# Kernel optimization log

Measured on AMD Instinct MI355X. Metric: run time of the kernel, lower is better.

Reference implementation:

```python
import jax, jax.numpy as jnp
import numpy as np

H = 2048  # hidden
D = 4     # bbox dims
B, T, TGT = 64, 128, 64


def lstm_cell(x, h, c, Wih, Whh, bih, bhh):
    # PyTorch gate order: i, f, g, o
    gates = x @ Wih.T + h @ Whh.T + bih + bhh  # (B, 4H)
    i, f, g, o = jnp.split(gates, 4, axis=-1)
    i = jax.nn.sigmoid(i)
    f = jax.nn.sigmoid(f)
    g = jnp.tanh(g)
    o = jax.nn.sigmoid(o)
    c_new = f * c + i * g
    h_new = o * jnp.tanh(c_new)
    return h_new, c_new


def setup_inputs() -> dict:
    key = jax.random.key(0)
    ks = jax.random.split(key, 16)
    x = jax.random.normal(ks[0], (B, T, D), dtype=jnp.float32)
    lengths = jax.random.randint(ks[1], (B,), 1, T + 1)  # valid lengths in [1, T]
    s = 1.0 / np.sqrt(H)

    def u(k, shape):
        return jax.random.uniform(k, shape, jnp.float32, -s, s)

    return dict(
        x=x, lengths=lengths, target_len=TGT,
        enc_Wih=u(ks[2], (4 * H, D)), enc_Whh=u(ks[3], (4 * H, H)),
        enc_bih=u(ks[4], (4 * H,)), enc_bhh=u(ks[5], (4 * H,)),
        emb_W=u(ks[6], (H, D)), emb_b=u(ks[7], (H,)),
        dec_Wih=u(ks[8], (4 * H, H)), dec_Whh=u(ks[9], (4 * H, H)),
        dec_bih=u(ks[10], (4 * H,)), dec_bhh=u(ks[11], (4 * H,)),
        fc_W=u(ks[12], (D, H)), fc_b=u(ks[13], (D,)),
    )


def reference(x, lengths, target_len,
              enc_Wih, enc_Whh, enc_bih, enc_bhh,
              emb_W, emb_b,
              dec_Wih, dec_Whh, dec_bih, dec_bhh,
              fc_W, fc_b):
    b, t, _ = x.shape
    # --- Encoder: LSTM over padded seq; packed semantics = freeze state past length ---
    mask = (jnp.arange(t)[:, None] < lengths[None, :])[:, :, None]  # (T, B, 1)
    xs = jnp.swapaxes(x, 0, 1)  # (T, B, D)
    h0 = jnp.zeros((b, H), x.dtype)
    c0 = jnp.zeros((b, H), x.dtype)

    def enc_step(carry, inp):
        h, c = carry
        xt, m = inp
        hn, cn = lstm_cell(xt, h, c, enc_Wih, enc_Whh, enc_bih, enc_bhh)
        return (jnp.where(m, hn, h), jnp.where(m, cn, c)), None

    (h, c), _ = jax.lax.scan(enc_step, (h0, c0), (xs, mask))

    x0 = x[jnp.arange(b), lengths - 1]  # (B, D)

    def dec_step(carry, _):
        xb, hh, cc = carry
        emb = xb @ emb_W.T + emb_b  # (B, H)
        hh, cc = lstm_cell(emb, hh, cc, dec_Wih, dec_Whh, dec_bih, dec_bhh)
        out = hh @ fc_W.T + fc_b  # (B, D)
        return (out, hh, cc), out

    (out, h, c), preds = jax.lax.scan(dec_step, (x0, h, c), None, length=target_len)
    predictions = jnp.swapaxes(preds, 0, 1)  # (B, target_len, D)
    # hidden returned with num_layers=1 leading axis, matching torch
    return predictions, out, (h[None], c[None])
```

## Files before the change

### kernel.cpp

```cpp
#include <hip/hip_runtime.h>
#include <hip/hip_fp16.h>


#define HID   2048
#define NBAT  64
#define TENC  128
#define TDEC  64
#define NBLK  256
#define NTHR  512
#define WROW  2056
#define FROW  2056

typedef _Float16 f16;
typedef _Float16 f16x8 __attribute__((ext_vector_type(8)));
typedef _Float16 f16x4 __attribute__((ext_vector_type(4)));
typedef float    f32x4v __attribute__((ext_vector_type(4)));

#define SMEM_BYTES 159936

#define DOT4(a,b) ((a).x*(b).x + (a).y*(b).y + (a).z*(b).z + (a).w*(b).w)

struct Params {
  const float* x; const int* lengths;
  const float* enc_Wih; const float* enc_Whh; const float* enc_bih; const float* enc_bhh;
  const float* emb_W; const float* emb_b;
  const float* dec_Wih; const float* dec_Whh; const float* dec_bih; const float* dec_bhh;
  const float* fc_W; const float* fc_b;
  float* dst;
  f16* h16;
  unsigned* bar;
  int ring;
};

__device__ __forceinline__ void astore_u64(f16* p, unsigned long long v) {
  __hip_atomic_store((unsigned long long*)p, v, __ATOMIC_RELAXED, __HIP_MEMORY_SCOPE_AGENT);
}
__device__ __forceinline__ f16x8 bload_f16x8(const f16* p) {
  f16x8 r;
  asm volatile("global_load_dwordx4 %0, %1, off sc0 sc1" : "=v"(r) : "v"(p));
  return r;
}
__device__ __forceinline__ void ldsbar() {
  asm volatile("s_waitcnt lgkmcnt(0)" ::: "memory");
  __builtin_amdgcn_s_barrier();
}
__device__ __forceinline__ void waitpa() {
  asm volatile("s_waitcnt vmcnt(0)" ::: "memory");
  __builtin_amdgcn_sched_barrier(0);
}

__device__ __forceinline__ void wait_slice(const unsigned* bar, int kq, int l,
                                           unsigned level) {
  const unsigned* slot = bar + (kq << 6) + l;
  for (;;) {
    unsigned v;
    asm volatile("global_load_dword %0, %1, off sc0 sc1\n\ts_waitcnt vmcnt(0)"
                 : "=v"(v) : "v"(slot) : "memory");
    if (v >= level) break;
    __builtin_amdgcn_s_sleep(1);
  }
}
__device__ __forceinline__ void arrive(unsigned* bar, int bid, unsigned level) {
  asm volatile("s_waitcnt vmcnt(0)" ::: "memory");
  asm volatile("global_store_dword %0, %1, off sc0 sc1\n\ts_waitcnt vmcnt(0)"
               :: "v"(bar + bid), "v"(level) : "memory");
}

__device__ __forceinline__ void fill_weights(const float* __restrict__ W, int bid,
                                             f16* wlds, int w, int l) {
  #pragma unroll
  for (int rr = 0; rr < 4; ++rr) {
    int r  = w * 4 + rr;
    int gr = ((r >> 3) << 11) + bid * 8 + (r & 7);
    const float4* src = (const float4*)(W + (size_t)gr * HID);
    f16* dst = wlds + (size_t)r * WROW;
    #pragma unroll
    for (int it = 0; it < 8; ++it) {
      float4 v = src[it * 64 + l];
      f16x4 h4; h4[0] = (f16)v.x; h4[1] = (f16)v.y; h4[2] = (f16)v.z; h4[3] = (f16)v.w;
      *(f16x4*)(dst + (it * 64 + l) * 4) = h4;
    }
  }
}

__device__ __forceinline__ void gemm_prefetch(const f16* __restrict__ hp, int ring,
                                              int w, int l15, int quad,
                                              f16x8* pa0, f16x8* pa1) {
  const int mh = w & 1, kq = w >> 1;
  const f16* A0 = hp + ((size_t)(kq * 64 + quad)) * 512 + (size_t)(mh * 32 + l15) * 8;
  if (ring) {
    #pragma unroll
    for (int ch = 0; ch < 16; ++ch) {
      pa0[ch] = *(const f16x8*)(A0 + ch * 2048);
      pa1[ch] = *(const f16x8*)(A0 + ch * 2048 + 128);
    }
  } else {
    #pragma unroll
    for (int ch = 0; ch < 16; ++ch) {
      pa0[ch] = bload_f16x8(A0 + ch * 2048);
      pa1[ch] = bload_f16x8(A0 + ch * 2048 + 128);
    }
  }
}

__device__ __forceinline__ void fc_compute(const f16* fcT, float* fcp,
                                           int w, int l15, int quad,
                                           const f16x8* pa0, const f16x8* pa1) {
  const int mh = w & 1, kq = w >> 1;
  f32x4v f0 = {0.f, 0.f, 0.f, 0.f}, f1 = f0;
  const f16* BF = fcT + (size_t)l15 * FROW + kq * 512 + quad * 8;
  #pragma unroll
  for (int ch = 0; ch < 16; ++ch) {
    f16x8 vbF = {};
    if (l15 < 4) vbF = *(const f16x8*)(BF + ch * 32);
    f0 = __builtin_amdgcn_mfma_f32_16x16x32_f16(pa0[ch], vbF, f0, 0, 0, 0);
    f1 = __builtin_amdgcn_mfma_f32_16x16x32_f16(pa1[ch], vbF, f1, 0, 0, 0);
  }
  if (l15 < 4) {
    const int brow = mh * 32 + quad * 4;
    #pragma unroll
    for (int r = 0; r < 4; ++r) {
      unsafeAtomicAdd(&fcp[(brow + r) * 4 + l15],      f0[r]);
      unsafeAtomicAdd(&fcp[(brow + 16 + r) * 4 + l15], f1[r]);
    }
  }
}

template<bool FC>
__device__ __forceinline__ void gemm_compute(const f16* wlds, const f16* fcT,
                                             float* gbuf, float* fcp,
                                             int w, int l15, int quad,
                                             const f16x8* pa0, const f16x8* pa1) {
  const int mh = w & 1, kq = w >> 1;
  f32x4v a00 = {0.f, 0.f, 0.f, 0.f}, a01 = a00, a10 = a00, a11 = a00;
  const f16* B0 = wlds + (size_t)l15 * WROW + kq * 512 + quad * 8;
  const f16* B1 = B0 + (size_t)16 * WROW;
  #pragma unroll
  for (int ch = 0; ch < 16; ++ch) {
    f16x8 vb0 = *(const f16x8*)(B0 + ch * 32);
    f16x8 vb1 = *(const f16x8*)(B1 + ch * 32);
    a00 = __builtin_amdgcn_mfma_f32_16x16x32_f16(pa0[ch], vb0, a00, 0, 0, 0);
    a01 = __builtin_amdgcn_mfma_f32_16x16x32_f16(pa0[ch], vb1, a01, 0, 0, 0);
    a10 = __builtin_amdgcn_mfma_f32_16x16x32_f16(pa1[ch], vb0, a10, 0, 0, 0);
    a11 = __builtin_amdgcn_mfma_f32_16x16x32_f16(pa1[ch], vb1, a11, 0, 0, 0);
  }
  const int brow = mh * 32 + quad * 4;
  #pragma unroll
  for (int r = 0; r < 4; ++r) {
    unsafeAtomicAdd(&gbuf[(brow + r)      * 36 +      l15], a00[r]);
    unsafeAtomicAdd(&gbuf[(brow + r)      * 36 + 16 + l15], a01[r]);
    unsafeAtomicAdd(&gbuf[(brow + 16 + r) * 36 +      l15], a10[r]);
    unsafeAtomicAdd(&gbuf[(brow + 16 + r) * 36 + 16 + l15], a11[r]);
  }
  if (FC) fc_compute(fcT, fcp, w, l15, quad, pa0, pa1);
}

extern "C" __global__ void __launch_bounds__(NTHR, 2)
lstm_persistent(Params P) {
  extern __shared__ char smem[];
  f16*   wlds = (f16*)smem;
  float* gbuf = (float*)(smem + 131584);
  float* xv   = (float*)(smem + 140800);
  float* wsm  = (float*)(smem + 141824);
  float* bsm  = (float*)(smem + 142336);
  float* fcp  = (float*)(smem + 142464);
  f16*   fcT  = (f16*)(smem + 143488);

  const int t    = threadIdx.x;
  const int bid  = blockIdx.x;
  const int w    = t >> 6;
  const int l    = t & 63;
  const int l15  = l & 15;
  const int quad = l >> 4;
  const int kq   = w >> 1;
  const int bb   = t >> 3;
  const int jj   = t & 7;
  const int jglob = bid * 8 + jj;
  const int ring = P.ring;
  const size_t GEN = (size_t)NBAT * HID;

  if (t == 0)
    asm volatile("s_waitcnt vmcnt(0)\n\tbuffer_inv sc0 sc1\n\ts_waitcnt vmcnt(0)" ::: "memory");
  __syncthreads();

  if (t < 32) {
    int r = t, gr = ((r >> 3) << 11) + bid * 8 + (r & 7);
    ((float4*)wsm)[r] = ((const float4*)P.enc_Wih)[gr];
    bsm[r] = P.enc_bih[gr] + P.enc_bhh[gr];
  }
  fill_weights(P.enc_Whh, bid, wlds, w, l);

  const int len_b = P.lengths[bb];
  const float4 fcb = ((const float4*)P.fc_b)[0];
  float hreg = 0.f, creg = 0.f;

  for (int ts = 0; ts < TENC; ++ts) {
    const size_t roff = (size_t)(ring ? ts : (ts & 1)) * GEN;
    const size_t woff = (size_t)(ring ? (ts + 1) : ((ts + 1) & 1)) * GEN;
    float4 xvv;
    if (t < NBAT) xvv = ((const float4*)P.x)[t * TENC + ts];
    for (int e = t; e < 2048; e += NTHR) {
      int b = e >> 5, n = e & 31;
      gbuf[b * 36 + n] = bsm[n];
    }
    if (t < NBAT) ((float4*)xv)[t] = xvv;
    ldsbar();
    if (ts > 0) {
      wait_slice(P.bar, kq, l, (unsigned)ts);
      f16x8 pa0[16], pa1[16];
      gemm_prefetch(P.h16 + roff, ring, w, l15, quad, pa0, pa1);
      if (!ring) waitpa();
      gemm_compute<false>(wlds, fcT, gbuf, fcp, w, l15, quad, pa0, pa1);
    }
    ldsbar();
    {
      const float4 xb  = ((const float4*)xv)[bb];
      const float4 wi4 = ((const float4*)wsm)[jj];
      const float4 wf4 = ((const float4*)wsm)[8 + jj];
      const float4 wg4 = ((const float4*)wsm)[16 + jj];
      const float4 wo4 = ((const float4*)wsm)[24 + jj];
      float gi = gbuf[bb * 36 + jj]      + DOT4(xb, wi4);
      float gf = gbuf[bb * 36 + 8 + jj]  + DOT4(xb, wf4);
      float gg = gbuf[bb * 36 + 16 + jj] + DOT4(xb, wg4);
      float go = gbuf[bb * 36 + 24 + jj] + DOT4(xb, wo4);
      float ii = 1.f / (1.f + expf(-gi));
      float ff = 1.f / (1.f + expf(-gf));
      float g  = tanhf(gg);
      float oo = 1.f / (1.f + expf(-go));
      float cn = ff * creg + ii * g;
      float hn = oo * tanhf(cn);
      if (ts < len_b) { creg = cn; hreg = hn; }
      unsigned hv = (unsigned)__builtin_bit_cast(unsigned short, (f16)hreg);
      unsigned v1 = __shfl_down(hv, 1), v2 = __shfl_down(hv, 2), v3 = __shfl_down(hv, 3);
      if ((t & 3) == 0) {
        unsigned long long pk = (unsigned long long)hv | ((unsigned long long)v1 << 16)
                              | ((unsigned long long)v2 << 32) | ((unsigned long long)v3 << 48);
        astore_u64(P.h16 + woff + (size_t)bid * 512 + (size_t)bb * 8 + (jj & 4), pk);
      }
    }
    __syncthreads();
    if (t == 0) arrive(P.bar, bid, (unsigned)(ts + 1));
  }

  fill_weights(P.dec_Whh, bid, wlds, w, l);
  #pragma unroll
  for (int rr = 0; rr < 4; ++rr) {
    int r = w * 4 + rr, gr = ((r >> 3) << 11) + bid * 8 + (r & 7);
    const float* wr = P.dec_Wih + (size_t)gr * HID;
    float a0 = 0.f, a1 = 0.f, a2 = 0.f, a3 = 0.f, ab = 0.f;
    for (int k = l; k < HID; k += 64) {
      float wv = wr[k];
      float4 e = ((const float4*)P.emb_W)[k];
      a0 += wv * e.x; a1 += wv * e.y; a2 += wv * e.z; a3 += wv * e.w;
      ab += wv * P.emb_b[k];
    }
    #pragma unroll
    for (int off = 32; off > 0; off >>= 1) {
      a0 += __shfl_xor(a0, off); a1 += __shfl_xor(a1, off);
      a2 += __shfl_xor(a2, off); a3 += __shfl_xor(a3, off);
      ab += __shfl_xor(ab, off);
    }
    if (l == 0) {
      wsm[r * 4 + 0] = a0; wsm[r * 4 + 1] = a1; wsm[r * 4 + 2] = a2; wsm[r * 4 + 3] = a3;
      bsm[r] = ab + P.dec_bih[gr] + P.dec_bhh[gr];
    }
  }
  for (int i = t; i < 2048; i += NTHR) {
    int d = i >> 9, k4 = i & 511;
    float4 v = ((const float4*)P.fc_W)[i];
    f16x4 h4; h4[0] = (f16)v.x; h4[1] = (f16)v.y; h4[2] = (f16)v.z; h4[3] = (f16)v.w;
    *(f16x4*)(fcT + (size_t)d * FROW + k4 * 4) = h4;
  }
  ldsbar();

  for (int s = 0; s < TDEC; ++s) {
    const int rgen = TENC + s, wgen = rgen + 1;
    const size_t roff = (size_t)(ring ? rgen : (rgen & 1)) * GEN;
    const size_t woff = (size_t)(ring ? wgen : (wgen & 1)) * GEN;
    if (t < 256) fcp[t] = 0.f;
    for (int e = t; e < 2048; e += NTHR) {
      int b = e >> 5, n = e & 31;
      gbuf[b * 36 + n] = bsm[n];
    }
    ldsbar();
    wait_slice(P.bar, kq, l, (unsigned)rgen);
    f16x8 pa0[16], pa1[16];
    gemm_prefetch(P.h16 + roff, ring, w, l15, quad, pa0, pa1);
    if (!ring) waitpa();
    gemm_compute<true>(wlds, fcT, gbuf, fcp, w, l15, quad, pa0, pa1);
    ldsbar();
    if (t < NBAT) {
      float4 o;
      if (s == 0) {
        o = ((const float4*)P.x)[t * TENC + (P.lengths[t] - 1)];
      } else {
        float4 p = ((const float4*)fcp)[t];
        o.x = fcb.x + p.x; o.y = fcb.y + p.y; o.z = fcb.z + p.z; o.w = fcb.w + p.w;
      }
      ((float4*)xv)[t] = o;
      if (s >= 1 && bid == s)
        ((float4*)P.dst)[t * TDEC + (s - 1)] = o;
    }
    ldsbar();
    {
      const float4 xb  = ((const float4*)xv)[bb];
      const float4 wi4 = ((const float4*)wsm)[jj];
      const float4 wf4 = ((const float4*)wsm)[8 + jj];
      const float4 wg4 = ((const float4*)wsm)[16 + jj];
      const float4 wo4 = ((const float4*)wsm)[24 + jj];
      float gi = gbuf[bb * 36 + jj]      + DOT4(xb, wi4);
      float gf = gbuf[bb * 36 + 8 + jj]  + DOT4(xb, wf4);
      float gg = gbuf[bb * 36 + 16 + jj] + DOT4(xb, wg4);
      float go = gbuf[bb * 36 + 24 + jj] + DOT4(xb, wo4);
      float ii = 1.f / (1.f + expf(-gi));
      float ff = 1.f / (1.f + expf(-gf));
      float g  = tanhf(gg);
      float oo = 1.f / (1.f + expf(-go));
      creg = ff * creg + ii * g;
      hreg = oo * tanhf(creg);
      unsigned hv = (unsigned)__builtin_bit_cast(unsigned short, (f16)hreg);
      unsigned v1 = __shfl_down(hv, 1), v2 = __shfl_down(hv, 2), v3 = __shfl_down(hv, 3);
      if ((t & 3) == 0) {
        unsigned long long pk = (unsigned long long)hv | ((unsigned long long)v1 << 16)
                              | ((unsigned long long)v2 << 32) | ((unsigned long long)v3 << 48);
        astore_u64(P.h16 + woff + (size_t)bid * 512 + (size_t)bb * 8 + (jj & 4), pk);
      }
    }
    __syncthreads();
    if (t == 0) arrive(P.bar, bid, (unsigned)wgen);
  }

  if (bid == 0) {
    wait_slice(P.bar, kq, l, (unsigned)(TENC + TDEC));
    if (t < 256) fcp[t] = 0.f;
    f16x8 pa0[16], pa1[16];
    gemm_prefetch(P.h16 + (size_t)(ring ? (TENC + TDEC) : ((TENC + TDEC) & 1)) * GEN,
                  ring, w, l15, quad, pa0, pa1);
    ldsbar();
    waitpa();
    fc_compute(fcT, fcp, w, l15, quad, pa0, pa1);
    ldsbar();
    if (t < NBAT) {
      float4 p = ((const float4*)fcp)[t];
      float4 o;
      o.x = fcb.x + p.x; o.y = fcb.y + p.y; o.z = fcb.z + p.z; o.w = fcb.w + p.w;
      ((float4*)P.dst)[t * TDEC + 63] = o;
      ((float4*)(P.dst + 16384))[t]   = o;
    }
  }
  P.dst[16640  + (size_t)bb * HID + jglob] = hreg;
  P.dst[147712 + (size_t)bb * HID + jglob] = creg;
}

extern "C" void kernel_launch(void* const* d_in, const int* in_sizes, int n_in,
                              void* d_out, int out_size, void* d_ws, size_t ws_size,
                              hipStream_t stream) {
  (void)in_sizes; (void)n_in; (void)out_size;
  Params P;
  P.x        = (const float*)d_in[0];
  P.lengths  = (const int*)  d_in[1];
  P.enc_Wih  = (const float*)d_in[3];
  P.enc_Whh  = (const float*)d_in[4];
  P.enc_bih  = (const float*)d_in[5];
  P.enc_bhh  = (const float*)d_in[6];
  P.emb_W    = (const float*)d_in[7];
  P.emb_b    = (const float*)d_in[8];
  P.dec_Wih  = (const float*)d_in[9];
  P.dec_Whh  = (const float*)d_in[10];
  P.dec_bih  = (const float*)d_in[11];
  P.dec_bhh  = (const float*)d_in[12];
  P.fc_W     = (const float*)d_in[13];
  P.fc_b     = (const float*)d_in[14];
  P.dst      = (float*)d_out;

  char* ws = (char*)d_ws;
  const size_t slot = (size_t)NBAT * HID * sizeof(_Float16);
  const size_t ring_bytes = (size_t)(TENC + TDEC + 1) * slot;
  int ring = (ws_size >= ring_bytes + 16384) ? 1 : 0;
  P.h16  = (f16*)ws;
  P.bar  = (unsigned*)(ws + (ring ? ring_bytes : 2 * slot));
  P.ring = ring;

  hipMemsetAsync(P.bar, 0, 12288, stream);

  hipFuncSetAttribute((const void*)lstm_persistent,
                      hipFuncAttributeMaxDynamicSharedMemorySize, SMEM_BYTES);
  void* args[] = { &P };
  hipLaunchCooperativeKernel((const void*)lstm_persistent, dim3(NBLK), dim3(NTHR),
                             args, SMEM_BYTES, stream);
}
```

Baseline: 3.491 ms.

## Add dedicated comms wavefront polling global barrier, publish readiness via LDS

Adds a ninth wavefront per block that polls the global per-block arrival counters with vectorized loads and ballots. It publishes per-slice readiness flags in LDS, and the compute waves spin on those flags instead of each polling global memory. The aim is to cut the global polling traffic and latency of the inter-block barrier on every timestep. In exchange it grows the block to 576 threads, changes launch bounds to one block per CU, and adds LDS spin loops.

```diff
diff --git a/kernel.cpp b/kernel.cpp
--- a/kernel.cpp
+++ b/kernel.cpp
@@ -7,7 +7,7 @@
 #define TENC  128
 #define TDEC  64
 #define NBLK  256
-#define NTHR  512
+#define NTHR  576
 #define WROW  2056
 #define FROW  2056
 
@@ -16,7 +16,7 @@
 typedef _Float16 f16x4 __attribute__((ext_vector_type(4)));
 typedef float    f32x4v __attribute__((ext_vector_type(4)));
 
-#define SMEM_BYTES 159936
+#define SMEM_BYTES 159952
 
 #define DOT4(a,b) ((a).x*(b).x + (a).y*(b).y + (a).z*(b).z + (a).w*(b).w)
 
@@ -40,6 +40,18 @@
   asm volatile("global_load_dwordx4 %0, %1, off sc0 sc1" : "=v"(r) : "v"(p));
   return r;
 }
+__device__ __forceinline__ uint4 aload_u32x4(const unsigned* p) {
+  uint4 r;
+  asm volatile("global_load_dwordx4 %0, %1, off sc0 sc1\n\ts_waitcnt vmcnt(0)"
+               : "=v"(r) : "v"(p) : "memory");
+  return r;
+}
+__device__ __forceinline__ int lds_ld(const int* p) {
+  return __hip_atomic_load(p, __ATOMIC_RELAXED, __HIP_MEMORY_SCOPE_WORKGROUP);
+}
+__device__ __forceinline__ void lds_st(int* p, int v) {
+  __hip_atomic_store(p, v, __ATOMIC_RELAXED, __HIP_MEMORY_SCOPE_WORKGROUP);
+}
 __device__ __forceinline__ void ldsbar() {
   asm volatile("s_waitcnt lgkmcnt(0)" ::: "memory");
   __builtin_amdgcn_s_barrier();
@@ -49,21 +61,32 @@
   __builtin_amdgcn_sched_barrier(0);
 }
 
-__device__ __forceinline__ void wait_slice(const unsigned* bar, int kq, int l,
-                                           unsigned level) {
-  const unsigned* slot = bar + (kq << 6) + l;
-  for (;;) {
-    unsigned v;
-    asm volatile("global_load_dword %0, %1, off sc0 sc1\n\ts_waitcnt vmcnt(0)"
-                 : "=v"(v) : "v"(slot) : "memory");
-    if (v >= level) break;
-    __builtin_amdgcn_s_sleep(1);
-  }
-}
 __device__ __forceinline__ void arrive(unsigned* bar, int bid, unsigned level) {
-  asm volatile("s_waitcnt vmcnt(0)" ::: "memory");
   asm volatile("global_store_dword %0, %1, off sc0 sc1\n\ts_waitcnt vmcnt(0)"
                :: "v"(bar + bid), "v"(level) : "memory");
+}
+__device__ __forceinline__ void comms_poll(const unsigned* bar, unsigned level,
+                                           int l, int* lds_lvl) {
+  const unsigned* slots = bar + l * 4;
+  unsigned pub = 0;
+  for (;;) {
+    uint4 v = aload_u32x4(slots);
+    int ok = (v.x >= level) & (v.y >= level) & (v.z >= level) & (v.w >= level);
+    unsigned long long bal = __ballot(ok);
+    #pragma unroll
+    for (int g = 0; g < 4; ++g) {
+      if (!(pub & (1u << g)) && ((bal >> (g * 16)) & 0xFFFFull) == 0xFFFFull) {
+        if (l == 0) lds_st(&lds_lvl[g], (int)level);
+        pub |= (1u << g);
+      }
+    }
+    if (pub == 0xFu) break;
+    __builtin_amdgcn_s_sleep(2);
+  }
+  asm volatile("s_waitcnt lgkmcnt(0)" ::: "memory");
+}
+__device__ __forceinline__ void spin_lds(const int* f, int level) {
+  while (lds_ld(f) < level) __builtin_amdgcn_s_sleep(1);
 }
 
 __device__ __forceinline__ void fill_weights(const float* __restrict__ W, int bid,
@@ -155,7 +178,7 @@
   if (FC) fc_compute(fcT, fcp, w, l15, quad, pa0, pa1);
 }
 
-extern "C" __global__ void __launch_bounds__(NTHR, 2)
+extern "C" __global__ void __launch_bounds__(NTHR, 1)
 lstm_persistent(Params P) {
   extern __shared__ char smem[];
   f16*   wlds = (f16*)smem;
@@ -165,22 +188,27 @@
   float* bsm  = (float*)(smem + 142336);
   float* fcp  = (float*)(smem + 142464);
   f16*   fcT  = (f16*)(smem + 143488);
+  int*   lds_lvl = (int*)(smem + 159936);
 
   const int t    = threadIdx.x;
   const int bid  = blockIdx.x;
   const int w    = t >> 6;
+  const bool cw  = (w == 8);
   const int l    = t & 63;
   const int l15  = l & 15;
   const int quad = l >> 4;
-  const int kq   = w >> 1;
+  const int kq   = (w >> 1) & 3;
   const int bb   = t >> 3;
   const int jj   = t & 7;
   const int jglob = bid * 8 + jj;
   const int ring = P.ring;
   const size_t GEN = (size_t)NBAT * HID;
 
-  if (t == 0)
+  if (t == 0) {
+    lds_st(&lds_lvl[0], 0); lds_st(&lds_lvl[1], 0);
+    lds_st(&lds_lvl[2], 0); lds_st(&lds_lvl[3], 0);
     asm volatile("s_waitcnt vmcnt(0)\n\tbuffer_inv sc0 sc1\n\ts_waitcnt vmcnt(0)" ::: "memory");
+  }
   __syncthreads();
 
   if (t < 32) {
@@ -188,9 +216,9 @@
     ((float4*)wsm)[r] = ((const float4*)P.enc_Wih)[gr];
     bsm[r] = P.enc_bih[gr] + P.enc_bhh[gr];
   }
-  fill_weights(P.enc_Whh, bid, wlds, w, l);
-
-  const int len_b = P.lengths[bb];
+  if (!cw) fill_weights(P.enc_Whh, bid, wlds, w, l);
+
+  const int len_b = cw ? 1 : P.lengths[bb];
   const float4 fcb = ((const float4*)P.fc_b)[0];
   float hreg = 0.f, creg = 0.f;
 
@@ -206,14 +234,18 @@
     if (t < NBAT) ((float4*)xv)[t] = xvv;
     ldsbar();
     if (ts > 0) {
-      wait_slice(P.bar, kq, l, (unsigned)ts);
-      f16x8 pa0[16], pa1[16];
-      gemm_prefetch(P.h16 + roff, ring, w, l15, quad, pa0, pa1);
-      if (!ring) waitpa();
-      gemm_compute<false>(wlds, fcT, gbuf, fcp, w, l15, quad, pa0, pa1);
-    }
-    ldsbar();
-    {
+      if (cw) {
+        comms_poll(P.bar, (unsigned)ts, l, lds_lvl);
+      } else {
+        spin_lds(lds_lvl + kq, ts);
+        f16x8 pa0[16], pa1[16];
+        gemm_prefetch(P.h16 + roff, ring, w, l15, quad, pa0, pa1);
+        if (!ring) waitpa();
+        gemm_compute<false>(wlds, fcT, gbuf, fcp, w, l15, quad, pa0, pa1);
+      }
+    }
+    ldsbar();
+    if (!cw) {
       const float4 xb  = ((const float4*)xv)[bb];
       const float4 wi4 = ((const float4*)wsm)[jj];
       const float4 wf4 = ((const float4*)wsm)[8 + jj];
@@ -242,27 +274,29 @@
     if (t == 0) arrive(P.bar, bid, (unsigned)(ts + 1));
   }
 
-  fill_weights(P.dec_Whh, bid, wlds, w, l);
-  #pragma unroll
-  for (int rr = 0; rr < 4; ++rr) {
-    int r = w * 4 + rr, gr = ((r >> 3) << 11) + bid * 8 + (r & 7);
-    const float* wr = P.dec_Wih + (size_t)gr * HID;
-    float a0 = 0.f, a1 = 0.f, a2 = 0.f, a3 = 0.f, ab = 0.f;
-    for (int k = l; k < HID; k += 64) {
-      float wv = wr[k];
-      float4 e = ((const float4*)P.emb_W)[k];
-      a0 += wv * e.x; a1 += wv * e.y; a2 += wv * e.z; a3 += wv * e.w;
-      ab += wv * P.emb_b[k];
-    }
-    #pragma unroll
-    for (int off = 32; off > 0; off >>= 1) {
-      a0 += __shfl_xor(a0, off); a1 += __shfl_xor(a1, off);
-      a2 += __shfl_xor(a2, off); a3 += __shfl_xor(a3, off);
-      ab += __shfl_xor(ab, off);
-    }
-    if (l == 0) {
-      wsm[r * 4 + 0] = a0; wsm[r * 4 + 1] = a1; wsm[r * 4 + 2] = a2; wsm[r * 4 + 3] = a3;
-      bsm[r] = ab + P.dec_bih[gr] + P.dec_bhh[gr];
+  if (!cw) {
+    fill_weights(P.dec_Whh, bid, wlds, w, l);
+    #pragma unroll
+    for (int rr = 0; rr < 4; ++rr) {
+      int r = w * 4 + rr, gr = ((r >> 3) << 11) + bid * 8 + (r & 7);
+      const float* wr = P.dec_Wih + (size_t)gr * HID;
+      float a0 = 0.f, a1 = 0.f, a2 = 0.f, a3 = 0.f, ab = 0.f;
+      for (int k = l; k < HID; k += 64) {
+        float wv = wr[k];
+        float4 e = ((const float4*)P.emb_W)[k];
+        a0 += wv * e.x; a1 += wv * e.y; a2 += wv * e.z; a3 += wv * e.w;
+        ab += wv * P.emb_b[k];
+      }
+      #pragma unroll
+      for (int off = 32; off > 0; off >>= 1) {
+        a0 += __shfl_xor(a0, off); a1 += __shfl_xor(a1, off);
+        a2 += __shfl_xor(a2, off); a3 += __shfl_xor(a3, off);
+        ab += __shfl_xor(ab, off);
+      }
+      if (l == 0) {
+        wsm[r * 4 + 0] = a0; wsm[r * 4 + 1] = a1; wsm[r * 4 + 2] = a2; wsm[r * 4 + 3] = a3;
+        bsm[r] = ab + P.dec_bih[gr] + P.dec_bhh[gr];
+      }
     }
   }
   for (int i = t; i < 2048; i += NTHR) {
@@ -283,11 +317,15 @@
       gbuf[b * 36 + n] = bsm[n];
     }
     ldsbar();
-    wait_slice(P.bar, kq, l, (unsigned)rgen);
-    f16x8 pa0[16], pa1[16];
-    gemm_prefetch(P.h16 + roff, ring, w, l15, quad, pa0, pa1);
-    if (!ring) waitpa();
-    gemm_compute<true>(wlds, fcT, gbuf, fcp, w, l15, quad, pa0, pa1);
+    if (cw) {
+      comms_poll(P.bar, (unsigned)rgen, l, lds_lvl);
+    } else {
+      spin_lds(lds_lvl + kq, rgen);
+      f16x8 pa0[16], pa1[16];
+      gemm_prefetch(P.h16 + roff, ring, w, l15, quad, pa0, pa1);
+      if (!ring) waitpa();
+      gemm_compute<true>(wlds, fcT, gbuf, fcp, w, l15, quad, pa0, pa1);
+    }
     ldsbar();
     if (t < NBAT) {
       float4 o;
@@ -302,7 +340,7 @@
         ((float4*)P.dst)[t * TDEC + (s - 1)] = o;
     }
     ldsbar();
-    {
+    if (!cw) {
       const float4 xb  = ((const float4*)xv)[bb];
       const float4 wi4 = ((const float4*)wsm)[jj];
       const float4 wf4 = ((const float4*)wsm)[8 + jj];
@@ -331,14 +369,16 @@
   }
 
   if (bid == 0) {
-    wait_slice(P.bar, kq, l, (unsigned)(TENC + TDEC));
+    if (cw) comms_poll(P.bar, (unsigned)(TENC + TDEC), l, lds_lvl);
+    else    spin_lds(lds_lvl + kq, TENC + TDEC);
     if (t < 256) fcp[t] = 0.f;
     f16x8 pa0[16], pa1[16];
-    gemm_prefetch(P.h16 + (size_t)(ring ? (TENC + TDEC) : ((TENC + TDEC) & 1)) * GEN,
-                  ring, w, l15, quad, pa0, pa1);
+    if (!cw)
+      gemm_prefetch(P.h16 + (size_t)(ring ? (TENC + TDEC) : ((TENC + TDEC) & 1)) * GEN,
+                    ring, w, l15, quad, pa0, pa1);
     ldsbar();
     waitpa();
-    fc_compute(fcT, fcp, w, l15, quad, pa0, pa1);
+    if (!cw) fc_compute(fcT, fcp, w, l15, quad, pa0, pa1);
     ldsbar();
     if (t < NBAT) {
       float4 p = ((const float4*)fcp)[t];
@@ -348,8 +388,10 @@
       ((float4*)(P.dst + 16384))[t]   = o;
     }
   }
-  P.dst[16640  + (size_t)bb * HID + jglob] = hreg;
-  P.dst[147712 + (size_t)bb * HID + jglob] = creg;
+  if (!cw) {
+    P.dst[16640  + (size_t)bb * HID + jglob] = hreg;
+    P.dst[147712 + (size_t)bb * HID + jglob] = creg;
+  }
 }
 
 extern "C" void kernel_launch(void* const* d_in, const int* in_sizes, int n_in,
```

Measured after the change: 3.522 ms. No clear change (+0.9%).
